# Kernel optimization log

Measured on AMD Instinct MI355X. Metric: run time of the kernel, lower is better.

The kernel has to match this reference:

```python
import jax, jax.numpy as jnp
import numpy as np
import math

B, L, HID = 2, 2048, 1024
NH, DH = 16, 64
MASK_VAL = -1000000000.0  # half_precision_flag == False


def setup_inputs() -> dict:
    key = jax.random.key(0)
    ks = jax.random.split(key, 12)
    s = 0.02
    return {
        "queries": jax.random.normal(ks[0], (B, L, HID), jnp.float32),
        "keys": jax.random.normal(ks[1], (B, L, HID), jnp.float32),
        "values": jax.random.normal(ks[2], (B, L, HID), jnp.float32),
        "mask": jax.random.randint(ks[3], (B, L, L), 0, 2, jnp.int32),
        "Wq": jax.random.normal(ks[4], (HID, NH * DH), jnp.float32) * s,
        "bq": jnp.zeros((NH * DH,), jnp.float32),
        "Wk": jax.random.normal(ks[5], (HID, NH * DH), jnp.float32) * s,
        "bk": jnp.zeros((NH * DH,), jnp.float32),
        "Wv": jax.random.normal(ks[6], (HID, NH * DH), jnp.float32) * s,
        "bv": jnp.zeros((NH * DH,), jnp.float32),
        "Wo": jax.random.normal(ks[7], (NH * DH, HID), jnp.float32) * s,
        "bo": jnp.zeros((HID,), jnp.float32),
    }


def reference(queries, keys, values, mask, Wq, bq, Wk, bk, Wv, bv, Wo, bo):
    # Linear projections: (B, L, NH*DH)
    q = queries @ Wq + bq
    k = keys @ Wk + bk
    v = values @ Wv + bv
    # FAITHFUL to original: raw .view(B, NH, -1, DH) without transpose
    q = q.reshape(B, NH, L, DH)
    k = k.reshape(B, NH, L, DH)
    v = v.reshape(B, NH, L, DH)
    # scaled dot-product scores: (B, NH, L, L)
    scores = jnp.einsum("bhqd,bhkd->bhqk", q, k) / math.sqrt(DH)
    scores = jnp.where(mask[:, None, :, :] == 0, MASK_VAL, scores)
    probs = jax.nn.softmax(scores, axis=-1)  # dropout p=0 -> identity
    ctx = jnp.einsum("bhqk,bhkd->bhqd", probs, v)  # (B, NH, L, DH)
    # transpose(1,2) then flatten heads, as in original
    ctx = ctx.transpose(0, 2, 1, 3).reshape(B, L, NH * DH)
    return ctx @ Wo + bo
```

## Files before the change

### kernel.cpp

```cpp
#include <hip/hip_runtime.h>
#include <stdint.h>

typedef __bf16 bf16;
typedef __bf16 bf16x8 __attribute__((ext_vector_type(8)));
typedef __bf16 bf16x4 __attribute__((ext_vector_type(4)));
typedef __bf16 bf16x2 __attribute__((ext_vector_type(2)));
typedef float  f32x4  __attribute__((ext_vector_type(4)));
typedef float  f32x16 __attribute__((ext_vector_type(16)));
typedef short  s16x4  __attribute__((ext_vector_type(4)));
typedef short  s16x8  __attribute__((ext_vector_type(8)));
typedef unsigned int u32x2 __attribute__((ext_vector_type(2)));
typedef unsigned int u32x4 __attribute__((ext_vector_type(4)));
typedef unsigned long long ull;

#define GLOAD16(gptr, lptr)                                                     \
  __builtin_amdgcn_global_load_lds(                                             \
      (const __attribute__((address_space(1))) void*)(gptr),                    \
      (__attribute__((address_space(3))) void*)(lptr), 16, 0, 0)

#define MFMA16(a, b, c) __builtin_amdgcn_mfma_f32_16x16x32_bf16((a), (b), (c), 0, 0, 0)
#define MFMA32(a, b, c) __builtin_amdgcn_mfma_f32_32x32x16_bf16((a), (b), (c), 0, 0, 0)

static constexpr int B_ = 2, L_ = 2048, NH_ = 16, DH_ = 64;
static constexpr float QSCALE = 0.18033688011112042f;

__global__ __launch_bounds__(256) void k_prep(const float* __restrict__ q,
                                              const float* __restrict__ k,
                                              const float* __restrict__ v,
                                              const int* __restrict__ mask,
                                              const float* __restrict__ wq,
                                              const float* __restrict__ wk,
                                              const float* __restrict__ wv,
                                              const float* __restrict__ wo,
                                              bf16* __restrict__ X,
                                              bf16* __restrict__ Wt,
                                              ull* __restrict__ mb) {
  __shared__ float t[32][33];
  const int bid = blockIdx.x, tid = threadIdx.x;
  if (bid < 2048) {
#pragma unroll
    for (int it = 0; it < 16; ++it) {
      int tt = (bid * 16 + it) * 256 + tid;
      ull bal = __ballot(mask[tt] != 0);
      if ((tid & 63) == 0) mb[tt >> 6] = bal;
    }
  } else if (bid < 4096) {
    const int u0 = (bid - 2048) * 6;
#pragma unroll
    for (int it = 0; it < 6; ++it) {
      int u = u0 + it;
      int z = u >> 12, x = u & 4095;
      const float* in = z == 0 ? q : (z == 1 ? k : v);
      bf16* out = X + (size_t)z * 4194304;
      int i = x * 256 + tid;
      const float4 f = ((const float4*)in)[i];
      bf16x4 o = {(bf16)f.x, (bf16)f.y, (bf16)f.z, (bf16)f.w};
      ((bf16x4*)out)[i] = o;
    }
  } else {
    const int t0 = (bid - 4096) * 4;
    for (int it = 0; it < 4; ++it) {
      int u = t0 + it;
      int z = u >> 10, rem = u & 1023;
      const float* in = z == 0 ? wq : (z == 1 ? wk : (z == 2 ? wv : wo));
      bf16* out = Wt + (size_t)z * 1048576;
      int bx = (rem & 31) * 32, by = (rem >> 5) * 32;
      int x = tid & 31, y = tid >> 5;
#pragma unroll
      for (int r = 0; r < 4; ++r)
        t[y + r * 8][x] = in[(size_t)(by + y + r * 8) * 1024 + bx + x];
      __syncthreads();
#pragma unroll
      for (int r = 0; r < 4; ++r)
        out[(size_t)(bx + y + r * 8) * 1024 + by + x] = (bf16)t[x][y + r * 8];
      __syncthreads();
    }
  }
}

__global__ __launch_bounds__(256) void k_gemm3(const bf16* __restrict__ Xb,
                                               const bf16* __restrict__ Wb,
                                               const float* __restrict__ b0,
                                               const float* __restrict__ b1,
                                               const float* __restrict__ b2,
                                               bf16* __restrict__ Ob) {
  const int z = blockIdx.z;
  const bf16* A  = Xb + (size_t)z * 4194304;
  const bf16* Bt = Wb + (size_t)z * 1048576;
  const float* bias = z == 0 ? b0 : (z == 1 ? b1 : b2);
  bf16* C = Ob + (size_t)z * 4194304;
  const int m0 = blockIdx.y * 128, n0 = blockIdx.x * 128;
  __shared__ __align__(16) bf16 As[128 * 32];
  __shared__ __align__(16) bf16 Bs[128 * 32];
  const int tid = threadIdx.x, lane = tid & 63, w = tid >> 6, quad = lane >> 4, l15 = lane & 15;
  const int wm = (w & 1) * 64, wn = (w >> 1) * 64;
  f32x4 acc[4][4] = {};
  for (int kt = 0; kt < 32; ++kt) {
    const int kk = kt * 32;
#pragma unroll
    for (int i = 0; i < 2; ++i) {
      int s = tid + i * 256;
      int r = s >> 2, c = (s & 3) ^ ((r >> 1) & 3);
      GLOAD16(A + (size_t)(m0 + r) * 1024 + kk + c * 8, As + s * 8);
      GLOAD16(Bt + (size_t)(n0 + r) * 1024 + kk + c * 8, Bs + s * 8);
    }
    __syncthreads();
    bf16x8 af[4], bb[4];
#pragma unroll
    for (int i = 0; i < 4; ++i) {
      int ra = wm + i * 16 + l15, rb = wn + i * 16 + l15;
      af[i] = *(const bf16x8*)(As + (ra * 4 + (quad ^ ((ra >> 1) & 3))) * 8);
      bb[i] = *(const bf16x8*)(Bs + (rb * 4 + (quad ^ ((rb >> 1) & 3))) * 8);
    }
#pragma unroll
    for (int mi = 0; mi < 4; ++mi)
#pragma unroll
      for (int ni = 0; ni < 4; ++ni)
        acc[mi][ni] = MFMA16(af[mi], bb[ni], acc[mi][ni]);
    __syncthreads();
  }
  const float scale = (z == 0) ? QSCALE : 1.0f;
#pragma unroll
  for (int mi = 0; mi < 4; ++mi)
#pragma unroll
    for (int ni = 0; ni < 4; ++ni) {
      int row = m0 + wm + mi * 16 + quad * 4;
      int col = n0 + wn + ni * 16 + l15;
      float bz = bias[col];
      if (z == 2) {
        int b_ = row >> 11, l = row & 2047;
        int hh = l >> 7;
        int i0 = (l & 127) * 16 + (col >> 6);
        int d  = col & 63;
        bf16* dst = C + (size_t)(b_ * 16 + hh) * 131072;
#pragma unroll
        for (int r = 0; r < 4; ++r) {
          int iK = i0 + 16 * r;
          dst[((size_t)(iK >> 3) * 64 + d) * 8 + (iK & 7)] = (bf16)(acc[mi][ni][r] + bz);
        }
      } else {
#pragma unroll
        for (int r = 0; r < 4; ++r)
          C[(size_t)(row + r) * 1024 + col] = (bf16)((acc[mi][ni][r] + bz) * scale);
      }
    }
}

__global__ __launch_bounds__(256) void k_gemmo(const bf16* __restrict__ A,
                                               const bf16* __restrict__ Bt,
                                               const float* __restrict__ bias,
                                               float* __restrict__ C) {
  const int m0 = blockIdx.y * 64, n0 = blockIdx.x * 128;
  __shared__ __align__(16) bf16 As[64 * 32];
  __shared__ __align__(16) bf16 Bs[128 * 32];
  const int tid = threadIdx.x, lane = tid & 63, w = tid >> 6, quad = lane >> 4, l15 = lane & 15;
  const int wn = w * 32;
  f32x4 acc[4][2] = {};
  for (int kt = 0; kt < 32; ++kt) {
    const int kk = kt * 32;
    {
      int r = tid >> 2, c = (tid & 3) ^ ((r >> 1) & 3);
      GLOAD16(A + (size_t)(m0 + r) * 1024 + kk + c * 8, As + tid * 8);
    }
#pragma unroll
    for (int i = 0; i < 2; ++i) {
      int s = tid + i * 256;
      int r = s >> 2, c = (s & 3) ^ ((r >> 1) & 3);
      GLOAD16(Bt + (size_t)(n0 + r) * 1024 + kk + c * 8, Bs + s * 8);
    }
    __syncthreads();
    bf16x8 af[4], bb[2];
#pragma unroll
    for (int i = 0; i < 4; ++i) {
      int ra = i * 16 + l15;
      af[i] = *(const bf16x8*)(As + (ra * 4 + (quad ^ ((ra >> 1) & 3))) * 8);
    }
#pragma unroll
    for (int i = 0; i < 2; ++i) {
      int rb = wn + i * 16 + l15;
      bb[i] = *(const bf16x8*)(Bs + (rb * 4 + (quad ^ ((rb >> 1) & 3))) * 8);
    }
#pragma unroll
    for (int mi = 0; mi < 4; ++mi)
#pragma unroll
      for (int ni = 0; ni < 2; ++ni)
        acc[mi][ni] = MFMA16(af[mi], bb[ni], acc[mi][ni]);
    __syncthreads();
  }
#pragma unroll
  for (int mi = 0; mi < 4; ++mi)
#pragma unroll
    for (int ni = 0; ni < 2; ++ni) {
      int row = m0 + mi * 16 + quad * 4;
      int col = n0 + wn + ni * 16 + l15;
      float bz = bias[col];
#pragma unroll
      for (int r = 0; r < 4; ++r)
        C[(size_t)(row + r) * 1024 + col] = acc[mi][ni][r] + bz;
    }
}

static __device__ __forceinline__ unsigned pack2(float a, float b) {
  bf16x2 t = {(bf16)a, (bf16)b};
  return __builtin_bit_cast(unsigned, t);
}

static __device__ __forceinline__ void flash_step(
    const bf16* __restrict__ Kc, const bf16* __restrict__ Vc, ull word,
    const bf16x8 (&qf)[4], bf16x8 ones8,
    int hi, int keyq, int swz, int vo0, int vo1, int vo2, int vo3,
    f32x16& accO0, f32x16& accO1, f32x16& accL) {
  bf16x8 v0 = *(const bf16x8*)(Vc + vo0);
  bf16x8 v1 = *(const bf16x8*)(Vc + vo1);
  bf16x8 v2 = *(const bf16x8*)(Vc + vo2);
  bf16x8 v3 = *(const bf16x8*)(Vc + vo3);

  f32x16 st = {};
  __builtin_amdgcn_s_setprio(1);
#pragma unroll
  for (int ks = 0; ks < 4; ++ks) {
    bf16x8 kf = *(const bf16x8*)(Kc + (keyq * 8 + ((ks * 2 + hi) ^ swz)) * 8);
    st = MFMA32(kf, qf[ks], st);
  }
  __builtin_amdgcn_s_setprio(0);

  const unsigned w32 = (unsigned)(word >> ((keyq & 32) + 4 * hi));
#pragma unroll
  for (int r = 0; r < 16; ++r) {
    const int bit = (r >> 2) * 8 + (r & 3);
    st[r] = (w32 >> bit) & 1u ? __builtin_amdgcn_exp2f(st[r]) : 0.f;
  }

  bf16x8 af0, af1;
  {
    unsigned c0 = pack2(st[0], st[1]);
    unsigned c1 = pack2(st[2], st[3]);
    unsigned c2 = pack2(st[4], st[5]);
    unsigned c3 = pack2(st[6], st[7]);
    u32x2 s0 = __builtin_amdgcn_permlane32_swap(c0, c2, false, false);
    u32x2 s1 = __builtin_amdgcn_permlane32_swap(c1, c3, false, false);
    u32x4 a4 = {s0.x, s1.x, s0.y, s1.y};
    af0 = __builtin_bit_cast(bf16x8, a4);
    c0 = pack2(st[8], st[9]);
    c1 = pack2(st[10], st[11]);
    c2 = pack2(st[12], st[13]);
    c3 = pack2(st[14], st[15]);
    s0 = __builtin_amdgcn_permlane32_swap(c0, c2, false, false);
    s1 = __builtin_amdgcn_permlane32_swap(c1, c3, false, false);
    u32x4 b4 = {s0.x, s1.x, s0.y, s1.y};
    af1 = __builtin_bit_cast(bf16x8, b4);
  }

  __builtin_amdgcn_s_setprio(1);
  accL  = MFMA32(af0, ones8, accL);
  accL  = MFMA32(af1, ones8, accL);
  accO0 = MFMA32(af0, v0, accO0);
  accO1 = MFMA32(af0, v1, accO1);
  accO0 = MFMA32(af1, v2, accO0);
  accO1 = MFMA32(af1, v3, accO1);
  __builtin_amdgcn_s_setprio(0);
}

__global__ __launch_bounds__(256, 4) void k_flash(const bf16* __restrict__ Qp,
                                                  const bf16* __restrict__ Kp,
                                                  const bf16* __restrict__ Vtp,
                                                  const ull* __restrict__ mb,
                                                  bf16* __restrict__ ctx) {
  const int b = blockIdx.z, h = blockIdx.y, q0 = blockIdx.x * 64;
  const size_t HEAD = 131072;
  const bf16* Q  = Qp  + ((size_t)b * NH_ + h) * HEAD;
  const bf16* K  = Kp  + ((size_t)b * NH_ + h) * HEAD;
  const bf16* Vt = Vtp + ((size_t)b * NH_ + h) * HEAD;
  const ull* mrow = mb + (size_t)b * L_ * 32;

  __shared__ __align__(16) unsigned char RAW[34816];
  bf16* Ksb = (bf16*)RAW;
  bf16* Vsb = (bf16*)(RAW + 16384);
  ull*  Msb = (ull*)(RAW + 32768);

  const int tid = threadIdx.x, lane = tid & 63, w = tid >> 6;
  const int hi = lane >> 5, l31 = lane & 31;
  const int kh = w & 1, qq = w >> 1;
  const int keyq = kh * 32 + l31;
  const int swz = (keyq ^ (keyq >> 3)) & 7;
  const int vo0 = ((kh * 4 + hi) * 64 + l31) * 8;
  const int vo1 = vo0 + 256;
  const int vo2 = vo0 + 1024;
  const int vo3 = vo2 + 256;

  bf16x8 qf[4];
  {
    const bf16* qrow = Q + (size_t)(q0 + qq * 32 + l31) * 64 + hi * 8;
    qf[0] = *(const bf16x8*)(qrow);
    qf[1] = *(const bf16x8*)(qrow + 16);
    qf[2] = *(const bf16x8*)(qrow + 32);
    qf[3] = *(const bf16x8*)(qrow + 48);
  }

#define STAGE(T, SL)                                                            \
  {                                                                             \
    _Pragma("unroll")                                                           \
    for (int i_ = 0; i_ < 2; ++i_) {                                            \
      int s_ = tid + i_ * 256;                                                  \
      int key_ = s_ >> 3, c_ = (s_ & 7) ^ ((key_ ^ (key_ >> 3)) & 7);           \
      GLOAD16(K + ((size_t)(T) * 64 + key_) * 64 + c_ * 8, Ksb + (SL) * 4096 + s_ * 8); \
      GLOAD16(Vt + (size_t)(T) * 4096 + s_ * 8, Vsb + (SL) * 4096 + s_ * 8);    \
    }                                                                           \
  }

  STAGE(0, 0);
  if (w == 0) GLOAD16(mrow + (size_t)(q0 + lane) * 32, (bf16*)Msb + lane * 8);
  __syncthreads();

  f32x16 accO0 = {}, accO1 = {}, accL = {};
  const s16x8 one8s = {0x3F80, 0x3F80, 0x3F80, 0x3F80, 0x3F80, 0x3F80, 0x3F80, 0x3F80};
  const bf16x8 ones8 = __builtin_bit_cast(bf16x8, one8s);

  for (int kt = 0; kt < 32; ++kt) {
    const int cur = kt & 1;
    if (kt + 1 < 32) {
      STAGE(kt + 1, cur ^ 1);
      if ((kt & 1) && w == 0)
        GLOAD16(mrow + (size_t)(q0 + lane) * 32 + (kt + 1),
                (bf16*)Msb + (((kt + 1) >> 1) & 1) * 512 + lane * 8);
    }
    const ull word = Msb[((kt >> 1) & 1) * 128 + (qq * 32 + l31) * 2 + cur];
    flash_step(Ksb + cur * 4096, Vsb + cur * 4096, word, qf, ones8, hi, keyq, swz,
               vo0, vo1, vo2, vo3, accO0, accO1, accL);
    __syncthreads();
  }
#undef STAGE

  float* red  = (float*)RAW;
  float* redL = (float*)(RAW + 16384);
  if (kh == 1) {
#pragma unroll
    for (int r = 0; r < 16; ++r) {
      const int qrel = (r & 3) + 8 * (r >> 2) + 4 * hi;
      red[qq * 2048 + qrel * 64 + l31]      = accO0[r];
      red[qq * 2048 + qrel * 64 + 32 + l31] = accO1[r];
      if (l31 == 0) redL[qq * 32 + qrel] = accL[r];
    }
  }
  __syncthreads();
  if (kh == 0) {
#pragma unroll
    for (int r = 0; r < 16; ++r) {
      const int qrel = (r & 3) + 8 * (r >> 2) + 4 * hi;
      const float ls = accL[r] + redL[qq * 32 + qrel];
      const float rl = 1.0f / ls;
      const float o0 = accO0[r] + red[qq * 2048 + qrel * 64 + l31];
      const float o1 = accO1[r] + red[qq * 2048 + qrel * 64 + 32 + l31];
      const int rowg = q0 + qq * 32 + qrel;
      ctx[((size_t)b * L_ + rowg) * 1024 + h * 64 + l31]      = (bf16)(o0 * rl);
      ctx[((size_t)b * L_ + rowg) * 1024 + h * 64 + 32 + l31] = (bf16)(o1 * rl);
    }
  }
}

extern "C" void kernel_launch(void* const* d_in, const int* in_sizes, int n_in,
                              void* d_out, int out_size, void* d_ws, size_t ws_size,
                              hipStream_t stream) {
  (void)in_sizes; (void)n_in; (void)out_size; (void)ws_size;
  const float* q    = (const float*)d_in[0];
  const float* k    = (const float*)d_in[1];
  const float* v    = (const float*)d_in[2];
  const int*   mask = (const int*)d_in[3];
  const float* Wq = (const float*)d_in[4];
  const float* bq = (const float*)d_in[5];
  const float* Wk = (const float*)d_in[6];
  const float* bk = (const float*)d_in[7];
  const float* Wv = (const float*)d_in[8];
  const float* bv = (const float*)d_in[9];
  const float* Wo = (const float*)d_in[10];
  const float* bo = (const float*)d_in[11];
  float* out = (float*)d_out;

  char* ws = (char*)d_ws;
  const size_t SX = (size_t)4096 * 1024 * 2;
  const size_t SW = (size_t)1024 * 1024 * 2;
  bf16* X   = (bf16*)(ws);
  bf16* Wt  = (bf16*)(ws + 3 * SX);
  bf16* QKV = (bf16*)(ws + 3 * SX + 4 * SW);
  bf16* Qp  = QKV;
  bf16* Kp  = QKV + 4194304;
  bf16* Vtp = QKV + 2 * 4194304;
  bf16* Ctx = (bf16*)(ws + 6 * SX + 4 * SW);
  ull* mbits = (ull*)(ws + 7 * SX + 4 * SW);

  dim3 blk(256);
  k_prep<<<5120, blk, 0, stream>>>(q, k, v, mask, Wq, Wk, Wv, Wo, X, Wt, mbits);

  k_gemm3<<<dim3(8, 32, 3), blk, 0, stream>>>(X, Wt, bq, bk, bv, QKV);

  k_flash<<<dim3(32, NH_, B_), blk, 0, stream>>>(Qp, Kp, Vtp, mbits, Ctx);

  k_gemmo<<<dim3(8, 64), blk, 0, stream>>>(Ctx, Wt + 3 * 1048576, bo, out);
}
```

Measured before the change: 266.5 us.

## Double flash block to 128 queries with 512 threads; swizzle GEMM block order

The flash kernel now handles 128 query rows per block with 8 waves, so each staged K/V tile is shared by twice as many queries and K/V traffic per query is halved. Each thread issues one staging load per tile instead of two. Mask loading is widened and now reads 32-bit words. Both GEMMs switch to a 1D grid with a grouped block ordering meant to improve L2 reuse of A and B tiles. The cost is fewer flash blocks, 512 in total, with larger per-block LDS and no occupancy hint, so latency hiding may suffer.

```diff
diff --git a/kernel.cpp b/kernel.cpp
--- a/kernel.cpp
+++ b/kernel.cpp
@@ -84,12 +84,15 @@
                                                const float* __restrict__ b1,
                                                const float* __restrict__ b2,
                                                bf16* __restrict__ Ob) {
-  const int z = blockIdx.z;
+  const int lin = blockIdx.x;
+  const int cx = lin & 7, j = (lin >> 3) & 7, gg = lin >> 6;
+  const int g = gg * 8 + cx;
+  const int y = g & 31, z = g >> 5;
+  const int m0 = y * 128, n0 = j * 128;
   const bf16* A  = Xb + (size_t)z * 4194304;
   const bf16* Bt = Wb + (size_t)z * 1048576;
   const float* bias = z == 0 ? b0 : (z == 1 ? b1 : b2);
   bf16* C = Ob + (size_t)z * 4194304;
-  const int m0 = blockIdx.y * 128, n0 = blockIdx.x * 128;
   __shared__ __align__(16) bf16 As[128 * 32];
   __shared__ __align__(16) bf16 Bs[128 * 32];
   const int tid = threadIdx.x, lane = tid & 63, w = tid >> 6, quad = lane >> 4, l15 = lane & 15;
@@ -150,7 +153,10 @@
                                                const bf16* __restrict__ Bt,
                                                const float* __restrict__ bias,
                                                float* __restrict__ C) {
-  const int m0 = blockIdx.y * 64, n0 = blockIdx.x * 128;
+  const int lin = blockIdx.x;
+  const int cx = lin & 7, j = (lin >> 3) & 7, gg = lin >> 6;
+  const int y = gg * 8 + cx;
+  const int m0 = y * 64, n0 = j * 128;
   __shared__ __align__(16) bf16 As[64 * 32];
   __shared__ __align__(16) bf16 Bs[128 * 32];
   const int tid = threadIdx.x, lane = tid & 63, w = tid >> 6, quad = lane >> 4, l15 = lane & 15;
@@ -206,7 +212,7 @@
 }
 
 static __device__ __forceinline__ void flash_step(
-    const bf16* __restrict__ Kc, const bf16* __restrict__ Vc, ull word,
+    const bf16* __restrict__ Kc, const bf16* __restrict__ Vc, unsigned mw32,
     const bf16x8 (&qf)[4], bf16x8 ones8,
     int hi, int keyq, int swz, int vo0, int vo1, int vo2, int vo3,
     f32x16& accO0, f32x16& accO1, f32x16& accL) {
@@ -224,11 +230,10 @@
   }
   __builtin_amdgcn_s_setprio(0);
 
-  const unsigned w32 = (unsigned)(word >> ((keyq & 32) + 4 * hi));
 #pragma unroll
   for (int r = 0; r < 16; ++r) {
     const int bit = (r >> 2) * 8 + (r & 3);
-    st[r] = (w32 >> bit) & 1u ? __builtin_amdgcn_exp2f(st[r]) : 0.f;
+    st[r] = (mw32 >> bit) & 1u ? __builtin_amdgcn_exp2f(st[r]) : 0.f;
   }
 
   bf16x8 af0, af1;
@@ -261,22 +266,23 @@
   __builtin_amdgcn_s_setprio(0);
 }
 
-__global__ __launch_bounds__(256, 4) void k_flash(const bf16* __restrict__ Qp,
-                                                  const bf16* __restrict__ Kp,
-                                                  const bf16* __restrict__ Vtp,
-                                                  const ull* __restrict__ mb,
-                                                  bf16* __restrict__ ctx) {
-  const int b = blockIdx.z, h = blockIdx.y, q0 = blockIdx.x * 64;
+__global__ __launch_bounds__(512) void k_flash(const bf16* __restrict__ Qp,
+                                               const bf16* __restrict__ Kp,
+                                               const bf16* __restrict__ Vtp,
+                                               const ull* __restrict__ mb,
+                                               bf16* __restrict__ ctx) {
+  const int b = blockIdx.z, h = blockIdx.y, q0 = blockIdx.x * 128;
   const size_t HEAD = 131072;
   const bf16* Q  = Qp  + ((size_t)b * NH_ + h) * HEAD;
   const bf16* K  = Kp  + ((size_t)b * NH_ + h) * HEAD;
   const bf16* Vt = Vtp + ((size_t)b * NH_ + h) * HEAD;
   const ull* mrow = mb + (size_t)b * L_ * 32;
 
-  __shared__ __align__(16) unsigned char RAW[34816];
+  __shared__ __align__(16) unsigned char RAW[36864];
   bf16* Ksb = (bf16*)RAW;
   bf16* Vsb = (bf16*)(RAW + 16384);
   ull*  Msb = (ull*)(RAW + 32768);
+  const unsigned* Ms32 = (const unsigned*)(RAW + 32768);
 
   const int tid = threadIdx.x, lane = tid & 63, w = tid >> 6;
   const int hi = lane >> 5, l31 = lane & 31;
@@ -299,17 +305,16 @@
 
 #define STAGE(T, SL)                                                            \
   {                                                                             \
-    _Pragma("unroll")                                                           \
-    for (int i_ = 0; i_ < 2; ++i_) {                                            \
-      int s_ = tid + i_ * 256;                                                  \
-      int key_ = s_ >> 3, c_ = (s_ & 7) ^ ((key_ ^ (key_ >> 3)) & 7);           \
-      GLOAD16(K + ((size_t)(T) * 64 + key_) * 64 + c_ * 8, Ksb + (SL) * 4096 + s_ * 8); \
-      GLOAD16(Vt + (size_t)(T) * 4096 + s_ * 8, Vsb + (SL) * 4096 + s_ * 8);    \
-    }                                                                           \
+    int s_ = tid, key_ = s_ >> 3, c_ = (s_ & 7) ^ ((key_ ^ (key_ >> 3)) & 7);   \
+    GLOAD16(K + ((size_t)(T) * 64 + key_) * 64 + c_ * 8, Ksb + (SL) * 4096 + s_ * 8); \
+    GLOAD16(Vt + (size_t)(T) * 4096 + s_ * 8, Vsb + (SL) * 4096 + s_ * 8);      \
   }
 
   STAGE(0, 0);
-  if (w == 0) GLOAD16(mrow + (size_t)(q0 + lane) * 32, (bf16*)Msb + lane * 8);
+  if (w < 2) {
+    int r = w * 64 + lane;
+    GLOAD16(mrow + (size_t)(q0 + r) * 32, (bf16*)Msb + r * 8);
+  }
   __syncthreads();
 
   f32x16 accO0 = {}, accO1 = {}, accL = {};
@@ -320,19 +325,22 @@
     const int cur = kt & 1;
     if (kt + 1 < 32) {
       STAGE(kt + 1, cur ^ 1);
-      if ((kt & 1) && w == 0)
-        GLOAD16(mrow + (size_t)(q0 + lane) * 32 + (kt + 1),
-                (bf16*)Msb + (((kt + 1) >> 1) & 1) * 512 + lane * 8);
-    }
-    const ull word = Msb[((kt >> 1) & 1) * 128 + (qq * 32 + l31) * 2 + cur];
-    flash_step(Ksb + cur * 4096, Vsb + cur * 4096, word, qf, ones8, hi, keyq, swz,
+      if ((kt & 1) && w < 2) {
+        int r = w * 64 + lane;
+        GLOAD16(mrow + (size_t)(q0 + r) * 32 + (kt + 1),
+                (bf16*)Msb + (((kt + 1) >> 1) & 1) * 1024 + r * 8);
+      }
+    }
+    const unsigned mw32 =
+        Ms32[((((kt >> 1) & 1) * 256 + (qq * 32 + l31) * 2 + cur) << 1) + kh] >> (4 * hi);
+    flash_step(Ksb + cur * 4096, Vsb + cur * 4096, mw32, qf, ones8, hi, keyq, swz,
                vo0, vo1, vo2, vo3, accO0, accO1, accL);
     __syncthreads();
   }
 #undef STAGE
 
   float* red  = (float*)RAW;
-  float* redL = (float*)(RAW + 16384);
+  float* redL = (float*)(RAW + 32768);
   if (kh == 1) {
 #pragma unroll
     for (int r = 0; r < 16; ++r) {
@@ -391,9 +399,9 @@
   dim3 blk(256);
   k_prep<<<5120, blk, 0, stream>>>(q, k, v, mask, Wq, Wk, Wv, Wo, X, Wt, mbits);
 
-  k_gemm3<<<dim3(8, 32, 3), blk, 0, stream>>>(X, Wt, bq, bk, bv, QKV);
-
-  k_flash<<<dim3(32, NH_, B_), blk, 0, stream>>>(Qp, Kp, Vtp, mbits, Ctx);
-
-  k_gemmo<<<dim3(8, 64), blk, 0, stream>>>(Ctx, Wt + 3 * 1048576, bo, out);
-}
+  k_gemm3<<<768, blk, 0, stream>>>(X, Wt, bq, bk, bv, QKV);
+
+  k_flash<<<dim3(16, NH_, B_), dim3(512), 0, stream>>>(Qp, Kp, Vtp, mbits, Ctx);
+
+  k_gemmo<<<512, blk, 0, stream>>>(Ctx, Wt + 3 * 1048576, bo, out);
+}
```

New measurement: 256.5 us. 1.04x faster.
